# Kernel tuning notes

Measured on AMD Instinct MI355X. Metric: run time of the kernel, lower is better.

The kernel has to match this reference:

```python
import jax, jax.numpy as jnp
import numpy as np
from jax import lax

B = 8; DIM = 256; NH = 8; PATCH = 8; WS = 28; STRIDE = 8; PAD = 14; ORF = 2.0; IMG = 448


def conv2d(x, w, stride, pad, groups=1):
    return lax.conv_general_dilated(
        x, w, (stride, stride), [(pad, pad), (pad, pad)],
        dimension_numbers=('NCHW', 'OIHW', 'NCHW'), feature_group_count=groups)


def ln_ch(x, g, b):
    # LayerNormProxy: LayerNorm over channel dim of NCHW
    m = jnp.mean(x, 1, keepdims=True)
    v = jnp.mean((x - m) ** 2, 1, keepdims=True)
    return (x - m) * lax.rsqrt(v + 1e-5) * g[None, :, None, None] + b[None, :, None, None]


def bilinear_sample(x, grid):
    # x: (N,C,H,W); grid: (N,Hg,Wg,2) in (x,y) order, [-1,1], align_corners=True, zeros padding
    N, C, H, W = x.shape
    gx = (grid[..., 0] + 1.0) * 0.5 * (W - 1)
    gy = (grid[..., 1] + 1.0) * 0.5 * (H - 1)
    x0 = jnp.floor(gx); y0 = jnp.floor(gy)
    x1 = x0 + 1.0; y1 = y0 + 1.0
    wx1 = gx - x0; wx0 = 1.0 - wx1
    wy1 = gy - y0; wy0 = 1.0 - wy1
    xf = x.reshape(N, C, H * W)

    def corner(ix, iy, w):
        valid = (ix >= 0) & (ix <= W - 1) & (iy >= 0) & (iy <= H - 1)
        ii = (jnp.clip(iy, 0, H - 1) * W + jnp.clip(ix, 0, W - 1)).astype(jnp.int32).reshape(N, -1)
        vals = jax.vmap(lambda f, i: f[:, i])(xf, ii)  # (N,C,Hg*Wg)
        return vals * (w * valid).reshape(N, 1, -1)

    out = (corner(x0, y0, wx0 * wy0) + corner(x1, y0, wx1 * wy0)
           + corner(x0, y1, wx0 * wy1) + corner(x1, y1, wx1 * wy1))
    return out.reshape(N, C, grid.shape[1], grid.shape[2])


def setup_inputs() -> dict:
    key = jax.random.key(0)
    ks = jax.random.split(key, 12)
    s = 0.02
    CG = 64
    return {
        'x': jax.random.normal(ks[0], (B, 3, IMG, IMG), jnp.float32),
        'patch_w': jax.random.normal(ks[1], (DIM, 3, PATCH, PATCH), jnp.float32) * s,
        'patch_b': jnp.zeros((DIM,), jnp.float32),
        'ln1_g': jnp.ones((DIM,), jnp.float32),
        'ln1_b': jnp.zeros((DIM,), jnp.float32),
        'wq': jax.random.normal(ks[2], (DIM, DIM), jnp.float32) * s,
        'bq': jnp.zeros((DIM,), jnp.float32),
        'wk': jax.random.normal(ks[3], (DIM, DIM), jnp.float32) * s,
        'bk': jnp.zeros((DIM,), jnp.float32),
        'wv': jax.random.normal(ks[4], (DIM, DIM), jnp.float32) * s,
        'bv': jnp.zeros((DIM,), jnp.float32),
        'wo': jax.random.normal(ks[5], (DIM, DIM), jnp.float32) * s,
        'bo': jnp.zeros((DIM,), jnp.float32),
        'off_dw_w': jax.random.normal(ks[6], (CG, 1, WS, WS), jnp.float32) * s,
        'off_dw_b': jnp.zeros((CG,), jnp.float32),
        'off_ln_g': jnp.ones((CG,), jnp.float32),
        'off_ln_b': jnp.zeros((CG,), jnp.float32),
        'off_pw_w': jax.random.normal(ks[7], (2, CG), jnp.float32) * s,
        'rpe_w1': jax.random.normal(ks[8], (32, 2), jnp.float32) * 0.1,
        'rpe_b1': jnp.zeros((32,), jnp.float32),
        'rpe_w2': jax.random.normal(ks[9], (2, 32), jnp.float32) * 0.1,
    }


def reference(x, patch_w, patch_b, ln1_g, ln1_b, wq, bq, wk, bk, wv, bv, wo, bo,
              off_dw_w, off_dw_b, off_ln_g, off_ln_b, off_pw_w, rpe_w1, rpe_b1, rpe_w2):
    Bn = x.shape[0]
    # patch embedding: Conv2d(3, dim, patch, patch) + LayerNormProxy
    feat = conv2d(x, patch_w, PATCH, 0) + patch_b[None, :, None, None]
    feat = ln_ch(feat, ln1_g, ln1_b)
    H, W = feat.shape[2], feat.shape[3]  # 56, 56
    G = (H // WS) * (W // WS)            # 4 groups
    CG = DIM // G; GH = NH // G; HC = DIM // NH
    # q projection (1x1 conv)
    q = jnp.einsum('oc,bchw->bohw', wq, feat) + bq[None, :, None, None]
    # offset network on per-group query features
    q_off = q.reshape(Bn * G, CG, H, W)
    off = conv2d(q_off, off_dw_w, STRIDE, PAD, groups=CG) + off_dw_b[None, :, None, None]
    off = jax.nn.gelu(ln_ch(off, off_ln_g, off_ln_b), approximate=False)
    off = jnp.einsum('oc,bchw->bohw', off_pw_w, off)   # (B*G, 2, Hk, Wk)
    Hk, Wk = off.shape[2], off.shape[3]
    ns = Hk * Wk
    rng = jnp.array([1.0 / (Hk - 1), 1.0 / (Wk - 1)], off.dtype).reshape(1, 2, 1, 1)
    offset = jnp.tanh(off) * rng * ORF
    offset = jnp.transpose(offset, (0, 2, 3, 1))  # (B*G, Hk, Wk, 2) in (y, x)
    # reference points, normalized to ~[-1, 1]
    ry = jnp.linspace(0.5, Hk - 0.5, Hk) / (Hk - 1) * 2.0 - 1.0
    rx = jnp.linspace(0.5, Wk - 0.5, Wk) / (Wk - 1) * 2.0 - 1.0
    ref = jnp.stack(jnp.meshgrid(ry, rx, indexing='ij'), -1)  # (Hk, Wk, 2)
    ref = jnp.broadcast_to(ref[None], (Bn * G, Hk, Wk, 2))
    pos = offset + ref
    # deformable sampling (grid expects (x, y) order)
    xs = bilinear_sample(feat.reshape(Bn * G, CG, H, W), pos[..., ::-1])  # (B*G, CG, Hk, Wk)
    xs = xs.reshape(Bn, DIM, ns)
    k = jnp.einsum('oc,bcn->bon', wk, xs) + bk[None, :, None]
    v = jnp.einsum('oc,bcn->bon', wv, xs) + bv[None, :, None]
    qh = q.reshape(Bn * NH, HC, H * W)
    kh = k.reshape(Bn * NH, HC, ns)
    vh = v.reshape(Bn * NH, HC, ns)
    attn = jnp.einsum('bcm,bcn->bmn', qh, kh) * (HC ** -0.5)  # (B*NH, HW, ns)
    # log-CPB relative position bias
    qy = jnp.linspace(0.0, float(H), H) / (H - 1) * 2.0 - 1.0
    qx = jnp.linspace(0.0, float(W), W) / (W - 1) * 2.0 - 1.0
    qg = jnp.stack(jnp.meshgrid(qy, qx, indexing='ij'), -1).reshape(H * W, 2)
    disp = (qg[None, :, None, :] - pos.reshape(Bn * G, ns, 2)[:, None, :, :]) * 4.0
    disp = jnp.sign(disp) * jnp.log2(jnp.abs(disp) + 1.0) / 3.0  # /log2(8)
    bias = jax.nn.relu(jnp.einsum('bmnc,hc->bmnh', disp, rpe_w1) + rpe_b1)
    bias = jnp.einsum('bmnh,oh->bmno', bias, rpe_w2)  # (B*G, HW, ns, GH)
    attn = attn + jnp.transpose(bias, (0, 3, 1, 2)).reshape(Bn * NH, H * W, ns)
    attn = jax.nn.softmax(attn, axis=-1)
    out = jnp.einsum('bmn,bcn->bcm', attn, vh).reshape(Bn, DIM, H, W)
    y = jnp.einsum('oc,bchw->bohw', wo, out) + bo[None, :, None, None]
    return (y, pos.reshape(Bn, G, Hk, Wk, 2), ref.reshape(Bn, G, Hk, Wk, 2))
```

## Files before the change

### kernel.cpp

```cpp
#include <hip/hip_runtime.h>
#include <cstddef>


typedef short bf16x8 __attribute__((ext_vector_type(8)));
typedef float f32x4 __attribute__((ext_vector_type(4)));

static __device__ __forceinline__ ushort f2bf(float f) {
  union { float f; unsigned u; } v; v.f = f;
  unsigned r = v.u + 0x7fffu + ((v.u >> 16) & 1u);
  return (ushort)(r >> 16);
}
static __device__ __forceinline__ float bf2f(ushort u) {
  union { unsigned u; float f; } v; v.u = ((unsigned)u) << 16;
  return v.f;
}

#define OFF_FEATB 0u
#define OFF_QPK   3211264u
#define OFF_Q     6422528u
#define OFF_POS   12845056u
#define OFF_XS    12849152u
#define OFF_KPK   12980224u
#define OFF_VPK   13045760u
#define OFF_PWP   13111296u
#define OFF_WQP   13135872u
#define OFF_WOP   13168640u
#define OFF_WKT   13201408u
#define OFF_WVT   13266944u

__global__ __launch_bounds__(256) void k_pack(
    const float* __restrict__ pw, const float* __restrict__ wq,
    const float* __restrict__ wk, const float* __restrict__ wv,
    const float* __restrict__ wo, ushort* __restrict__ pwp,
    ushort* __restrict__ wqp, ushort* __restrict__ wop,
    float* __restrict__ wkT, float* __restrict__ wvT) {
  const int o = blockIdx.x, t = threadIdx.x, m = blockIdx.y;
  if (m == 0) {
    if (t < 192) pwp[((t >> 3) * 256 + o) * 8 + (t & 7)] = f2bf(pw[o * 192 + t]);
  } else if (m == 1) {
    wqp[((t >> 3) * 256 + o) * 8 + (t & 7)] = f2bf(wq[o * 256 + t]);
  } else if (m == 2) {
    wop[((t >> 3) * 256 + o) * 8 + (t & 7)] = f2bf(wo[o * 256 + t]);
  } else if (m == 3) {
    wkT[t * 256 + o] = wk[o * 256 + t];
  } else {
    wvT[t * 256 + o] = wv[o * 256 + t];
  }
}

__global__ __launch_bounds__(256) void k_patch_mfma(
    const float* __restrict__ x, const ushort* __restrict__ pwp,
    const float* __restrict__ pb, const float* __restrict__ g1,
    const float* __restrict__ b1, ushort* __restrict__ featb) {
  const int t = threadIdx.x;
  const int lane = t & 63;
  const int wid = t >> 6;
  const int m_base = blockIdx.x * 64 + wid * 16;
  const int kg = lane >> 4;
  const int lr = lane & 15;
  const int mA = m_base + lr;
  const int bA = mA / 3136;
  const int posA = mA - bA * 3136;
  const int ohA = posA / 56;
  const int owA = posA - ohA * 56;

  f32x4 acc[16];
#pragma unroll
  for (int f = 0; f < 16; f++) {
    float bv = pb[f * 16 + lr];
    acc[f] = (f32x4){bv, bv, bv, bv};
  }
#pragma unroll
  for (int ks = 0; ks < 6; ks++) {
    const int k8 = ks * 4 + kg;
    const int ci = k8 >> 3, ii = k8 & 7;
    const float* xp =
        x + (((size_t)bA * 3 + ci) * 448 + (ohA * 8 + ii)) * 448 + owA * 8;
    float4 v0 = *(const float4*)xp;
    float4 v1 = *(const float4*)(xp + 4);
    bf16x8 a;
    a[0] = (short)f2bf(v0.x); a[1] = (short)f2bf(v0.y);
    a[2] = (short)f2bf(v0.z); a[3] = (short)f2bf(v0.w);
    a[4] = (short)f2bf(v1.x); a[5] = (short)f2bf(v1.y);
    a[6] = (short)f2bf(v1.z); a[7] = (short)f2bf(v1.w);
#pragma unroll
    for (int f = 0; f < 16; f++) {
      bf16x8 bfr = *(const bf16x8*)(pwp + (size_t)(k8 * 256 + f * 16 + lr) * 8);
      acc[f] = __builtin_amdgcn_mfma_f32_16x16x32_bf16(a, bfr, acc[f], 0, 0, 0);
    }
  }
  float mean[4], rstd[4];
#pragma unroll
  for (int j = 0; j < 4; j++) {
    float s1 = 0.f, s2 = 0.f;
#pragma unroll
    for (int f = 0; f < 16; f++) { float v = acc[f][j]; s1 += v; s2 += v * v; }
#pragma unroll
    for (int off = 8; off >= 1; off >>= 1) {
      s1 += __shfl_xor(s1, off);
      s2 += __shfl_xor(s2, off);
    }
    float mn = s1 * (1.f / 256.f);
    float var = s2 * (1.f / 256.f) - mn * mn;
    mean[j] = mn; rstd[j] = rsqrtf(var + 1e-5f);
  }
#pragma unroll
  for (int f = 0; f < 16; f++) {
    const int c = f * 16 + lr;
    const float gg = g1[c], bb = b1[c];
#pragma unroll
    for (int j = 0; j < 4; j++) {
      const int mo = m_base + kg * 4 + j;
      float v = (acc[f][j] - mean[j]) * rstd[j] * gg + bb;
      featb[(size_t)mo * 256 + c] = f2bf(v);
    }
  }
}

__global__ __launch_bounds__(512) void k_gemm_mfma(
    const ushort* __restrict__ apk, const ushort* __restrict__ wp,
    const float* __restrict__ bias, float* __restrict__ out,
    ushort* __restrict__ opk) {
  const int t = threadIdx.x;
  const int lane = t & 63;
  const int wid = t >> 6;
  const int mt = wid >> 1, nh = wid & 1;
  const int lr = lane & 15, kg = lane >> 4;
  const int m_base = blockIdx.x * 64 + mt * 16;
  const int mA = m_base + lr;

  f32x4 acc[8];
#pragma unroll
  for (int f = 0; f < 8; f++) {
    float bv = bias[nh * 128 + f * 16 + lr];
    acc[f] = (f32x4){bv, bv, bv, bv};
  }
  const ushort* arow = apk + (size_t)mA * 256;
#pragma unroll
  for (int ks = 0; ks < 8; ks++) {
    bf16x8 a = *(const bf16x8*)(arow + ks * 32 + kg * 8);
#pragma unroll
    for (int f = 0; f < 8; f++) {
      const int o = nh * 128 + f * 16 + lr;
      bf16x8 bfr = *(const bf16x8*)(wp + (size_t)((ks * 4 + kg) * 256 + o) * 8);
      acc[f] = __builtin_amdgcn_mfma_f32_16x16x32_bf16(a, bfr, acc[f], 0, 0, 0);
    }
  }
  __shared__ float sA[64 * 257];
#pragma unroll
  for (int f = 0; f < 8; f++) {
#pragma unroll
    for (int j = 0; j < 4; j++)
      sA[(mt * 16 + kg * 4 + j) * 257 + nh * 128 + f * 16 + lr] = acc[f][j];
  }
  __syncthreads();
  const int b = (blockIdx.x * 64) / 3136;
  const int pos0 = (blockIdx.x * 64) % 3136;
#pragma unroll
  for (int i = 0; i < 32; i++) {
    int idx = t + i * 512;
    int c = idx >> 6, mm = idx & 63;
    out[((size_t)b * 256 + c) * 3136 + pos0 + mm] = sA[mm * 257 + c];
  }
  if (opk) {
    const int mm = t & 63;
    const int cs = t >> 6;
#pragma unroll
    for (int i = 0; i < 4; i++) {
      int c0 = cs * 32 + i * 8;
      bf16x8 v8;
#pragma unroll
      for (int j = 0; j < 8; j++) v8[j] = (short)f2bf(sA[mm * 257 + c0 + j]);
      *(bf16x8*)(opk + ((size_t)(blockIdx.x * 64 + mm)) * 256 + c0) = v8;
    }
  }
}

__global__ __launch_bounds__(128) void k_offset_conv(
    const float* __restrict__ q, const float* __restrict__ dww,
    float* __restrict__ convo) {
  const int bg = blockIdx.y;
  const int wv = threadIdx.x >> 6;
  const int lane = threadIdx.x & 63;
  const int ch = blockIdx.x * 2 + wv;
  const int b = bg >> 2, g = bg & 3;

  __shared__ float pl[2][7072];
  float* P = pl[wv];
  for (int idx = lane; idx < 7072; idx += 64) P[idx] = 0.f;

  const float* qb = q + ((size_t)b * 256 + g * 64 + ch) * 3136;
  if (lane < 56) {
    for (int r = 0; r < 56; r++) {
      int hr = r + 14;
      P[hr * 84 + (lane + 14) + (hr >> 3)] = qb[r * 56 + lane];
    }
  }
  const int oh = lane >> 3, ow = lane & 7;
  const int chs = __builtin_amdgcn_readfirstlane(ch);
  const float* wr = dww + (size_t)chs * 784;
  float acc = 0.f;
  const int r0 = oh * 8, c0 = ow * 8;
  for (int i = 0; i < 28; i++) {
    int hr = r0 + i;
    const float* prow = P + hr * 84 + c0 + (hr >> 3);
    const float* wrr = wr + i * 28;
#pragma unroll
    for (int j = 0; j < 28; j++)
      acc = fmaf(prow[j], wrr[j], acc);
  }
  convo[bg * 4096 + lane * 64 + ch] = acc;
}

__global__ __launch_bounds__(256) void k_offset_post(
    const float* __restrict__ convo, const float* __restrict__ dwb,
    const float* __restrict__ lng, const float* __restrict__ lnb,
    const float* __restrict__ pww, float* __restrict__ pos_ws,
    float* __restrict__ out_pos, float* __restrict__ out_ref) {
  const int bg = blockIdx.y;
  const int wv = threadIdx.x >> 6;
  const int lane = threadIdx.x & 63;
  const int idx = blockIdx.x * 4 + wv;
  const int oh = idx >> 3, ow = idx & 7;

  float acc = convo[bg * 4096 + idx * 64 + lane] + dwb[lane];

  float s1 = acc, s2 = acc * acc;
#pragma unroll
  for (int off = 32; off >= 1; off >>= 1) {
    s1 += __shfl_xor(s1, off);
    s2 += __shfl_xor(s2, off);
  }
  float m = s1 * (1.f / 64.f);
  float var = s2 * (1.f / 64.f) - m * m;
  float val = (acc - m) * rsqrtf(var + 1e-5f) * lng[lane] + lnb[lane];
  val = 0.5f * val * (1.f + erff(val * 0.70710678118654752f));
  float p0 = pww[lane] * val, p1 = pww[64 + lane] * val;
#pragma unroll
  for (int off = 32; off >= 1; off >>= 1) {
    p0 += __shfl_xor(p0, off);
    p1 += __shfl_xor(p1, off);
  }
  if (lane == 0) {
    float offy = tanhf(p0) * (2.0f / 7.0f);
    float offx = tanhf(p1) * (2.0f / 7.0f);
    float ry = (0.5f + oh) * (2.0f / 7.0f) - 1.0f;
    float rx = (0.5f + ow) * (2.0f / 7.0f) - 1.0f;
    float py = offy + ry, px = offx + rx;
    int o = bg * 128 + idx * 2;
    pos_ws[o] = py;  pos_ws[o + 1] = px;
    out_pos[o] = py; out_pos[o + 1] = px;
    out_ref[o] = ry; out_ref[o + 1] = rx;
  }
}

__global__ __launch_bounds__(256) void k_sample(
    const ushort* __restrict__ featb, const float* __restrict__ pos_ws,
    float* __restrict__ xs) {
  const int bg = blockIdx.y;
  const int wv = threadIdx.x >> 6, lane = threadIdx.x & 63;
  const int n = blockIdx.x * 4 + wv;
  const int b = bg >> 2, g = bg & 3;

  float py = pos_ws[bg * 128 + n * 2];
  float px = pos_ws[bg * 128 + n * 2 + 1];
  float gx = (px + 1.f) * 0.5f * 55.f;
  float gy = (py + 1.f) * 0.5f * 55.f;
  float x0f = floorf(gx), y0f = floorf(gy);
  int x0 = (int)x0f, y0 = (int)y0f;
  float wx1 = gx - x0f, wx0 = 1.f - wx1;
  float wy1 = gy - y0f, wy0 = 1.f - wy1;

  const size_t mb = (size_t)b * 3136;
  const int cofs = g * 64 + lane;
  float acc = 0.f;
  if (x0 >= 0 && x0 <= 55 && y0 >= 0 && y0 <= 55)
    acc = fmaf(bf2f(featb[(mb + y0 * 56 + x0) * 256 + cofs]), wx0 * wy0, acc);
  if (x0 + 1 >= 0 && x0 + 1 <= 55 && y0 >= 0 && y0 <= 55)
    acc = fmaf(bf2f(featb[(mb + y0 * 56 + x0 + 1) * 256 + cofs]), wx1 * wy0, acc);
  if (x0 >= 0 && x0 <= 55 && y0 + 1 >= 0 && y0 + 1 <= 55)
    acc = fmaf(bf2f(featb[(mb + (y0 + 1) * 56 + x0) * 256 + cofs]), wx0 * wy1, acc);
  if (x0 + 1 >= 0 && x0 + 1 <= 55 && y0 + 1 >= 0 && y0 + 1 <= 55)
    acc = fmaf(bf2f(featb[(mb + (y0 + 1) * 56 + x0 + 1) * 256 + cofs]), wx1 * wy1, acc);

  xs[((size_t)bg * 64 + lane) * 64 + n] = acc;
}

__global__ __launch_bounds__(256) void k_kv(
    const float* __restrict__ xs, const float* __restrict__ wkT,
    const float* __restrict__ bk, const float* __restrict__ wvT,
    const float* __restrict__ bv, ushort* __restrict__ kpk,
    ushort* __restrict__ vpk) {
  const int b = blockIdx.y;
  const int n = blockIdx.x;
  const int t = threadIdx.x;
  __shared__ float sxs[256];
  sxs[t] = xs[((size_t)b * 256 + t) * 64 + n];
  __syncthreads();
  float ak = bk[t], av = bv[t];
  for (int c = 0; c < 256; c++) {
    float xv = sxs[c];
    ak = fmaf(wkT[c * 256 + t], xv, ak);
    av = fmaf(wvT[c * 256 + t], xv, av);
  }
  const int h = t >> 5, cc = t & 31;
  const size_t base = (size_t)(b * 8 + h) * 2048;
  kpk[base + (size_t)((cc >> 3) * 64 + n) * 8 + (cc & 7)] = f2bf(ak);
  vpk[base + (size_t)((n >> 3) * 32 + cc) * 8 + (n & 7)] = f2bf(av);
}

__global__ __launch_bounds__(256) void k_attn_mfma(
    const ushort* __restrict__ qpk, const ushort* __restrict__ kpk,
    const ushort* __restrict__ vpk, const float* __restrict__ pos_ws,
    const float* __restrict__ w1, const float* __restrict__ b1,
    const float* __restrict__ w2, ushort* __restrict__ attnpk) {
  const int bg = blockIdx.y;
  const int b = bg >> 2, g = bg & 3;
  const int m0 = blockIdx.x * 64;
  const int t = threadIdx.x;
  const int lane = t & 63, w = t >> 6;

  __shared__ float bias0[64 * 68];
  __shared__ float bias1[64 * 68];
  __shared__ ushort Pbuf[4][16 * 72];
  __shared__ float posl[128];
  __shared__ float4 rpe4[32];
  __shared__ float rpeB[32];

  if (t < 128) posl[t] = pos_ws[bg * 128 + t];
  if (t < 32) {
    rpe4[t] = make_float4(w1[t * 2], w1[t * 2 + 1], b1[t], w2[t]);
    rpeB[t] = w2[32 + t];
  }
  __syncthreads();

  {
    const int i = t >> 2;
    const int n0 = (t & 3) * 16;
    const int m = m0 + i;
    const int my = m / 56, mx = m % 56;
    const float qgy = (float)my * (56.0f / 55.0f) * (2.0f / 55.0f) - 1.0f;
    const float qgx = (float)mx * (56.0f / 55.0f) * (2.0f / 55.0f) - 1.0f;
    float ty[16], tx[16], a0[16], a1[16];
#pragma unroll
    for (int u = 0; u < 16; u++) {
      int n = n0 + u;
      float dy = (qgy - posl[2 * n]) * 4.f;
      float dx = (qgx - posl[2 * n + 1]) * 4.f;
      ty[u] = copysignf(log2f(fabsf(dy) + 1.f) * (1.f / 3.f), dy);
      tx[u] = copysignf(log2f(fabsf(dx) + 1.f) * (1.f / 3.f), dx);
      a0[u] = 0.f; a1[u] = 0.f;
    }
    for (int j = 0; j < 32; j++) {
      float4 r = rpe4[j];
      float wb = rpeB[j];
#pragma unroll
      for (int u = 0; u < 16; u++) {
        float hv = fmaf(r.x, ty[u], fmaf(r.y, tx[u], r.z));
        hv = fmaxf(hv, 0.f);
        a0[u] = fmaf(r.w, hv, a0[u]);
        a1[u] = fmaf(wb, hv, a1[u]);
      }
    }
    float* b0p = bias0 + i * 68 + n0;
    float* b1p = bias1 + i * 68 + n0;
#pragma unroll
    for (int u = 0; u < 16; u++) { b0p[u] = a0[u]; b1p[u] = a1[u]; }
  }

  const int lr = lane & 15, kg = lane >> 4;
  const int mrow = m0 + w * 16 + lr;
  const float scale = 0.17677669529663687f;
  ushort* pb = Pbuf[w];

  f32x4 oacc[2][2];
#pragma unroll
  for (int gh = 0; gh < 2; gh++)
#pragma unroll
    for (int cf = 0; cf < 2; cf++) oacc[gh][cf] = (f32x4){0.f, 0.f, 0.f, 0.f};

#pragma unroll
  for (int gh = 0; gh < 2; gh++) {
    bf16x8 a = *(const bf16x8*)(qpk +
        ((size_t)(b * 3136 + mrow) * 256 + g * 64 + gh * 32 + kg * 8));
    const ushort* kbase = kpk + (size_t)(b * 8 + g * 2 + gh) * 2048;
    f32x4 s[4];
#pragma unroll
    for (int nf = 0; nf < 4; nf++) {
      bf16x8 bfr = *(const bf16x8*)(kbase + (size_t)(kg * 64 + nf * 16 + lr) * 8);
      s[nf] = __builtin_amdgcn_mfma_f32_16x16x32_bf16(
          a, bfr, (f32x4){0.f, 0.f, 0.f, 0.f}, 0, 0, 0);
    }
    const float* bt = gh ? bias1 : bias0;
#pragma unroll
    for (int nf = 0; nf < 4; nf++)
#pragma unroll
      for (int j = 0; j < 4; j++)
        s[nf][j] = fmaf(s[nf][j], scale,
                        bt[(w * 16 + kg * 4 + j) * 68 + nf * 16 + lr]);
#pragma unroll
    for (int j = 0; j < 4; j++) {
      float m1 = fmaxf(fmaxf(s[0][j], s[1][j]), fmaxf(s[2][j], s[3][j]));
#pragma unroll
      for (int o = 8; o >= 1; o >>= 1) m1 = fmaxf(m1, __shfl_xor(m1, o));
      float ss = 0.f;
#pragma unroll
      for (int nf = 0; nf < 4; nf++) {
        float e = __expf(s[nf][j] - m1);
        s[nf][j] = e;
        ss += e;
      }
#pragma unroll
      for (int o = 8; o >= 1; o >>= 1) ss += __shfl_xor(ss, o);
      float inv = 1.f / ss;
#pragma unroll
      for (int nf = 0; nf < 4; nf++) s[nf][j] *= inv;
    }
#pragma unroll
    for (int nf = 0; nf < 4; nf++)
#pragma unroll
      for (int j = 0; j < 4; j++)
        pb[(kg * 4 + j) * 72 + nf * 16 + lr] = f2bf(s[nf][j]);
    const ushort* vbase = vpk + (size_t)(b * 8 + g * 2 + gh) * 2048;
#pragma unroll
    for (int ks = 0; ks < 2; ks++) {
      bf16x8 pa = *(const bf16x8*)(pb + lr * 72 + ks * 32 + kg * 8);
#pragma unroll
      for (int cf = 0; cf < 2; cf++) {
        bf16x8 vb = *(const bf16x8*)(vbase +
            (size_t)((ks * 4 + kg) * 32 + cf * 16 + lr) * 8);
        oacc[gh][cf] = __builtin_amdgcn_mfma_f32_16x16x32_bf16(
            pa, vb, oacc[gh][cf], 0, 0, 0);
      }
    }
  }

  ushort* outb = (ushort*)bias0;
#pragma unroll
  for (int gh = 0; gh < 2; gh++)
#pragma unroll
    for (int cf = 0; cf < 2; cf++)
#pragma unroll
      for (int j = 0; j < 4; j++)
        outb[(w * 16 + kg * 4 + j) * 136 + gh * 32 + cf * 16 + lr] =
            f2bf(oacc[gh][cf][j]);
  __syncthreads();
#pragma unroll
  for (int r2 = 0; r2 < 2; r2++) {
    int row = (t >> 3) + r2 * 32;
    int chunk = t & 7;
    bf16x8 v8 = *(const bf16x8*)(outb + row * 136 + chunk * 8);
    *(bf16x8*)(attnpk +
               ((size_t)(b * 3136 + m0 + row) * 256 + g * 64 + chunk * 8)) = v8;
  }
}

extern "C" void kernel_launch(void* const* d_in, const int* in_sizes, int n_in,
                              void* d_out, int out_size, void* d_ws,
                              size_t ws_size, hipStream_t stream) {
  const float* x       = (const float*)d_in[0];
  const float* patch_w = (const float*)d_in[1];
  const float* patch_b = (const float*)d_in[2];
  const float* ln1_g   = (const float*)d_in[3];
  const float* ln1_b   = (const float*)d_in[4];
  const float* wq      = (const float*)d_in[5];
  const float* bq      = (const float*)d_in[6];
  const float* wk      = (const float*)d_in[7];
  const float* bk      = (const float*)d_in[8];
  const float* wv      = (const float*)d_in[9];
  const float* bv      = (const float*)d_in[10];
  const float* wo      = (const float*)d_in[11];
  const float* bo      = (const float*)d_in[12];
  const float* off_dw_w = (const float*)d_in[13];
  const float* off_dw_b = (const float*)d_in[14];
  const float* off_ln_g = (const float*)d_in[15];
  const float* off_ln_b = (const float*)d_in[16];
  const float* off_pw_w = (const float*)d_in[17];
  const float* rpe_w1  = (const float*)d_in[18];
  const float* rpe_b1  = (const float*)d_in[19];
  const float* rpe_w2  = (const float*)d_in[20];

  float* ws = (float*)d_ws;
  ushort* featb = (ushort*)(ws + OFF_FEATB);
  ushort* attnpk = featb;
  ushort* qpk = (ushort*)(ws + OFF_QPK);
  float* q    = ws + OFF_Q;
  float* posw = ws + OFF_POS;
  float* xs   = ws + OFF_XS;
  float* convo = ws + OFF_XS;
  ushort* kpk = (ushort*)(ws + OFF_KPK);
  ushort* vpk = (ushort*)(ws + OFF_VPK);
  ushort* pwp = (ushort*)(ws + OFF_PWP);
  ushort* wqp = (ushort*)(ws + OFF_WQP);
  ushort* wop = (ushort*)(ws + OFF_WOP);
  float* wkT  = ws + OFF_WKT;
  float* wvT  = ws + OFF_WVT;

  float* y = (float*)d_out;
  float* out_pos = y + 6422528;
  float* out_ref = out_pos + 4096;

  hipLaunchKernelGGL(k_pack, dim3(256, 5), dim3(256), 0, stream,
                     patch_w, wq, wk, wv, wo, pwp, wqp, wop, wkT, wvT);
  hipLaunchKernelGGL(k_patch_mfma, dim3(392), dim3(256), 0, stream,
                     x, pwp, patch_b, ln1_g, ln1_b, featb);
  hipLaunchKernelGGL(k_gemm_mfma, dim3(392), dim3(512), 0, stream,
                     featb, wqp, bq, q, qpk);
  hipLaunchKernelGGL(k_offset_conv, dim3(32, 32), dim3(128), 0, stream,
                     q, off_dw_w, convo);
  hipLaunchKernelGGL(k_offset_post, dim3(16, 32), dim3(256), 0, stream,
                     convo, off_dw_b, off_ln_g, off_ln_b, off_pw_w,
                     posw, out_pos, out_ref);
  hipLaunchKernelGGL(k_sample, dim3(16, 32), dim3(256), 0, stream,
                     featb, posw, xs);
  hipLaunchKernelGGL(k_kv, dim3(64, 8), dim3(256), 0, stream,
                     xs, wkT, bk, wvT, bv, kpk, vpk);
  hipLaunchKernelGGL(k_attn_mfma, dim3(49, 32), dim3(256), 0, stream,
                     qpk, kpk, vpk, posw, rpe_w1, rpe_b1, rpe_w2, attnpk);
  hipLaunchKernelGGL(k_gemm_mfma, dim3(392), dim3(512), 0, stream,
                     attnpk, wop, bo, y, (ushort*)nullptr);
}
```

Before: 240.0 us.

## Pre-convert input to bf16, fuse sampling into KV, compute RPE bias in registers

Three changes. A new pass converts the fp32 input image to bf16 once, so the patch-embed kernel reads half the bytes and drops its per-tile conversion, at the cost of an extra kernel plus a full write and read of the bf16 copy. The bilinear sampling kernel is merged into the K/V projection kernel, which removes the xs round trip through global memory and one launch. The attention kernel now computes the log-CPB bias in MFMA-fragment layout in registers with fast log2 instead of staging it in LDS, which cuts shared memory use but raises register pressure.

```diff
diff --git a/kernel.cpp b/kernel.cpp
--- a/kernel.cpp
+++ b/kernel.cpp
@@ -27,6 +27,19 @@
 #define OFF_WOP   13168640u
 #define OFF_WKT   13201408u
 #define OFF_WVT   13266944u
+
+__global__ __launch_bounds__(256) void k_xcvt(
+    const float* __restrict__ x, ushort* __restrict__ xb) {
+  const size_t i0 = ((size_t)blockIdx.x * 256 + threadIdx.x) * 8;
+  float4 v0 = *(const float4*)(x + i0);
+  float4 v1 = *(const float4*)(x + i0 + 4);
+  bf16x8 o;
+  o[0] = (short)f2bf(v0.x); o[1] = (short)f2bf(v0.y);
+  o[2] = (short)f2bf(v0.z); o[3] = (short)f2bf(v0.w);
+  o[4] = (short)f2bf(v1.x); o[5] = (short)f2bf(v1.y);
+  o[6] = (short)f2bf(v1.z); o[7] = (short)f2bf(v1.w);
+  *(bf16x8*)(xb + i0) = o;
+}
 
 __global__ __launch_bounds__(256) void k_pack(
     const float* __restrict__ pw, const float* __restrict__ wq,
@@ -49,7 +62,7 @@
 }
 
 __global__ __launch_bounds__(256) void k_patch_mfma(
-    const float* __restrict__ x, const ushort* __restrict__ pwp,
+    const ushort* __restrict__ xb, const ushort* __restrict__ pwp,
     const float* __restrict__ pb, const float* __restrict__ g1,
     const float* __restrict__ b1, ushort* __restrict__ featb) {
   const int t = threadIdx.x;
@@ -74,15 +87,8 @@
   for (int ks = 0; ks < 6; ks++) {
     const int k8 = ks * 4 + kg;
     const int ci = k8 >> 3, ii = k8 & 7;
-    const float* xp =
-        x + (((size_t)bA * 3 + ci) * 448 + (ohA * 8 + ii)) * 448 + owA * 8;
-    float4 v0 = *(const float4*)xp;
-    float4 v1 = *(const float4*)(xp + 4);
-    bf16x8 a;
-    a[0] = (short)f2bf(v0.x); a[1] = (short)f2bf(v0.y);
-    a[2] = (short)f2bf(v0.z); a[3] = (short)f2bf(v0.w);
-    a[4] = (short)f2bf(v1.x); a[5] = (short)f2bf(v1.y);
-    a[6] = (short)f2bf(v1.z); a[7] = (short)f2bf(v1.w);
+    bf16x8 a = *(const bf16x8*)(xb +
+        (((size_t)bA * 3 + ci) * 448 + (ohA * 8 + ii)) * 448 + owA * 8);
 #pragma unroll
     for (int f = 0; f < 16; f++) {
       bf16x8 bfr = *(const bf16x8*)(pwp + (size_t)(k8 * 256 + f * 16 + lr) * 8);
@@ -254,49 +260,42 @@
   }
 }
 
-__global__ __launch_bounds__(256) void k_sample(
+__global__ __launch_bounds__(256) void k_sample_kv(
     const ushort* __restrict__ featb, const float* __restrict__ pos_ws,
-    float* __restrict__ xs) {
-  const int bg = blockIdx.y;
-  const int wv = threadIdx.x >> 6, lane = threadIdx.x & 63;
-  const int n = blockIdx.x * 4 + wv;
-  const int b = bg >> 2, g = bg & 3;
-
-  float py = pos_ws[bg * 128 + n * 2];
-  float px = pos_ws[bg * 128 + n * 2 + 1];
-  float gx = (px + 1.f) * 0.5f * 55.f;
-  float gy = (py + 1.f) * 0.5f * 55.f;
-  float x0f = floorf(gx), y0f = floorf(gy);
-  int x0 = (int)x0f, y0 = (int)y0f;
-  float wx1 = gx - x0f, wx0 = 1.f - wx1;
-  float wy1 = gy - y0f, wy0 = 1.f - wy1;
-
-  const size_t mb = (size_t)b * 3136;
-  const int cofs = g * 64 + lane;
-  float acc = 0.f;
-  if (x0 >= 0 && x0 <= 55 && y0 >= 0 && y0 <= 55)
-    acc = fmaf(bf2f(featb[(mb + y0 * 56 + x0) * 256 + cofs]), wx0 * wy0, acc);
-  if (x0 + 1 >= 0 && x0 + 1 <= 55 && y0 >= 0 && y0 <= 55)
-    acc = fmaf(bf2f(featb[(mb + y0 * 56 + x0 + 1) * 256 + cofs]), wx1 * wy0, acc);
-  if (x0 >= 0 && x0 <= 55 && y0 + 1 >= 0 && y0 + 1 <= 55)
-    acc = fmaf(bf2f(featb[(mb + (y0 + 1) * 56 + x0) * 256 + cofs]), wx0 * wy1, acc);
-  if (x0 + 1 >= 0 && x0 + 1 <= 55 && y0 + 1 >= 0 && y0 + 1 <= 55)
-    acc = fmaf(bf2f(featb[(mb + (y0 + 1) * 56 + x0 + 1) * 256 + cofs]), wx1 * wy1, acc);
-
-  xs[((size_t)bg * 64 + lane) * 64 + n] = acc;
-}
-
-__global__ __launch_bounds__(256) void k_kv(
-    const float* __restrict__ xs, const float* __restrict__ wkT,
-    const float* __restrict__ bk, const float* __restrict__ wvT,
-    const float* __restrict__ bv, ushort* __restrict__ kpk,
-    ushort* __restrict__ vpk) {
+    const float* __restrict__ wkT, const float* __restrict__ bk,
+    const float* __restrict__ wvT, const float* __restrict__ bv,
+    ushort* __restrict__ kpk, ushort* __restrict__ vpk) {
   const int b = blockIdx.y;
   const int n = blockIdx.x;
   const int t = threadIdx.x;
+  const int g = t >> 6, lane = t & 63;
+  const int bg = b * 4 + g;
+
   __shared__ float sxs[256];
-  sxs[t] = xs[((size_t)b * 256 + t) * 64 + n];
+  {
+    float py = pos_ws[bg * 128 + n * 2];
+    float px = pos_ws[bg * 128 + n * 2 + 1];
+    float gx = (px + 1.f) * 0.5f * 55.f;
+    float gy = (py + 1.f) * 0.5f * 55.f;
+    float x0f = floorf(gx), y0f = floorf(gy);
+    int x0 = (int)x0f, y0 = (int)y0f;
+    float wx1 = gx - x0f, wx0 = 1.f - wx1;
+    float wy1 = gy - y0f, wy0 = 1.f - wy1;
+    const size_t mb = (size_t)b * 3136;
+    const int cofs = g * 64 + lane;
+    float acc = 0.f;
+    if (x0 >= 0 && x0 <= 55 && y0 >= 0 && y0 <= 55)
+      acc = fmaf(bf2f(featb[(mb + y0 * 56 + x0) * 256 + cofs]), wx0 * wy0, acc);
+    if (x0 + 1 >= 0 && x0 + 1 <= 55 && y0 >= 0 && y0 <= 55)
+      acc = fmaf(bf2f(featb[(mb + y0 * 56 + x0 + 1) * 256 + cofs]), wx1 * wy0, acc);
+    if (x0 >= 0 && x0 <= 55 && y0 + 1 >= 0 && y0 + 1 <= 55)
+      acc = fmaf(bf2f(featb[(mb + (y0 + 1) * 56 + x0) * 256 + cofs]), wx0 * wy1, acc);
+    if (x0 + 1 >= 0 && x0 + 1 <= 55 && y0 + 1 >= 0 && y0 + 1 <= 55)
+      acc = fmaf(bf2f(featb[(mb + (y0 + 1) * 56 + x0 + 1) * 256 + cofs]), wx1 * wy1, acc);
+    sxs[g * 64 + lane] = acc;
+  }
   __syncthreads();
+
   float ak = bk[t], av = bv[t];
   for (int c = 0; c < 256; c++) {
     float xv = sxs[c];
@@ -319,10 +318,10 @@
   const int m0 = blockIdx.x * 64;
   const int t = threadIdx.x;
   const int lane = t & 63, w = t >> 6;
-
-  __shared__ float bias0[64 * 68];
-  __shared__ float bias1[64 * 68];
+  const int lr = lane & 15, kg = lane >> 4;
+
   __shared__ ushort Pbuf[4][16 * 72];
+  __shared__ ushort outb[64 * 72];
   __shared__ float posl[128];
   __shared__ float4 rpe4[32];
   __shared__ float rpeB[32];
@@ -334,41 +333,41 @@
   }
   __syncthreads();
 
-  {
-    const int i = t >> 2;
-    const int n0 = (t & 3) * 16;
-    const int m = m0 + i;
-    const int my = m / 56, mx = m % 56;
-    const float qgy = (float)my * (56.0f / 55.0f) * (2.0f / 55.0f) - 1.0f;
-    const float qgx = (float)mx * (56.0f / 55.0f) * (2.0f / 55.0f) - 1.0f;
-    float ty[16], tx[16], a0[16], a1[16];
-#pragma unroll
-    for (int u = 0; u < 16; u++) {
-      int n = n0 + u;
-      float dy = (qgy - posl[2 * n]) * 4.f;
-      float dx = (qgx - posl[2 * n + 1]) * 4.f;
-      ty[u] = copysignf(log2f(fabsf(dy) + 1.f) * (1.f / 3.f), dy);
-      tx[u] = copysignf(log2f(fabsf(dx) + 1.f) * (1.f / 3.f), dx);
-      a0[u] = 0.f; a1[u] = 0.f;
-    }
-    for (int j = 0; j < 32; j++) {
-      float4 r = rpe4[j];
-      float wb = rpeB[j];
-#pragma unroll
-      for (int u = 0; u < 16; u++) {
-        float hv = fmaf(r.x, ty[u], fmaf(r.y, tx[u], r.z));
-        hv = fmaxf(hv, 0.f);
-        a0[u] = fmaf(r.w, hv, a0[u]);
-        a1[u] = fmaf(wb, hv, a1[u]);
-      }
-    }
-    float* b0p = bias0 + i * 68 + n0;
-    float* b1p = bias1 + i * 68 + n0;
-#pragma unroll
-    for (int u = 0; u < 16; u++) { b0p[u] = a0[u]; b1p[u] = a1[u]; }
-  }
-
-  const int lr = lane & 15, kg = lane >> 4;
+  float qgy[4], qgx[4];
+#pragma unroll
+  for (int j = 0; j < 4; j++) {
+    int m = m0 + w * 16 + kg * 4 + j;
+    int my = m / 56, mx = m % 56;
+    qgy[j] = (float)my * (56.0f / 55.0f) * (2.0f / 55.0f) - 1.0f;
+    qgx[j] = (float)mx * (56.0f / 55.0f) * (2.0f / 55.0f) - 1.0f;
+  }
+  float tyv[16], txv[16];
+#pragma unroll
+  for (int nf = 0; nf < 4; nf++) {
+    int n = nf * 16 + lr;
+    float py = posl[2 * n], px = posl[2 * n + 1];
+#pragma unroll
+    for (int j = 0; j < 4; j++) {
+      float dy = (qgy[j] - py) * 4.f;
+      float dx = (qgx[j] - px) * 4.f;
+      tyv[nf * 4 + j] = copysignf(__log2f(fabsf(dy) + 1.f) * (1.f / 3.f), dy);
+      txv[nf * 4 + j] = copysignf(__log2f(fabsf(dx) + 1.f) * (1.f / 3.f), dx);
+    }
+  }
+  float bb0[16], bb1[16];
+#pragma unroll
+  for (int p = 0; p < 16; p++) { bb0[p] = 0.f; bb1[p] = 0.f; }
+  for (int jj = 0; jj < 32; jj++) {
+    float4 r = rpe4[jj];
+    float wb = rpeB[jj];
+#pragma unroll
+    for (int p = 0; p < 16; p++) {
+      float hv = fmaxf(fmaf(r.x, tyv[p], fmaf(r.y, txv[p], r.z)), 0.f);
+      bb0[p] = fmaf(r.w, hv, bb0[p]);
+      bb1[p] = fmaf(wb, hv, bb1[p]);
+    }
+  }
+
   const int mrow = m0 + w * 16 + lr;
   const float scale = 0.17677669529663687f;
   ushort* pb = Pbuf[w];
@@ -391,13 +390,12 @@
       s[nf] = __builtin_amdgcn_mfma_f32_16x16x32_bf16(
           a, bfr, (f32x4){0.f, 0.f, 0.f, 0.f}, 0, 0, 0);
     }
-    const float* bt = gh ? bias1 : bias0;
 #pragma unroll
     for (int nf = 0; nf < 4; nf++)
 #pragma unroll
       for (int j = 0; j < 4; j++)
         s[nf][j] = fmaf(s[nf][j], scale,
-                        bt[(w * 16 + kg * 4 + j) * 68 + nf * 16 + lr]);
+                        gh ? bb1[nf * 4 + j] : bb0[nf * 4 + j]);
 #pragma unroll
     for (int j = 0; j < 4; j++) {
       float m1 = fmaxf(fmaxf(s[0][j], s[1][j]), fmaxf(s[2][j], s[3][j]));
@@ -435,21 +433,20 @@
     }
   }
 
-  ushort* outb = (ushort*)bias0;
 #pragma unroll
   for (int gh = 0; gh < 2; gh++)
 #pragma unroll
     for (int cf = 0; cf < 2; cf++)
 #pragma unroll
       for (int j = 0; j < 4; j++)
-        outb[(w * 16 + kg * 4 + j) * 136 + gh * 32 + cf * 16 + lr] =
+        outb[(w * 16 + kg * 4 + j) * 72 + gh * 32 + cf * 16 + lr] =
             f2bf(oacc[gh][cf][j]);
   __syncthreads();
 #pragma unroll
   for (int r2 = 0; r2 < 2; r2++) {
     int row = (t >> 3) + r2 * 32;
     int chunk = t & 7;
-    bf16x8 v8 = *(const bf16x8*)(outb + row * 136 + chunk * 8);
+    bf16x8 v8 = *(const bf16x8*)(outb + row * 72 + chunk * 8);
     *(bf16x8*)(attnpk +
                ((size_t)(b * 3136 + m0 + row) * 256 + g * 64 + chunk * 8)) = v8;
   }
@@ -485,8 +482,8 @@
   ushort* attnpk = featb;
   ushort* qpk = (ushort*)(ws + OFF_QPK);
   float* q    = ws + OFF_Q;
+  ushort* xb  = (ushort*)(ws + OFF_Q);
   float* posw = ws + OFF_POS;
-  float* xs   = ws + OFF_XS;
   float* convo = ws + OFF_XS;
   ushort* kpk = (ushort*)(ws + OFF_KPK);
   ushort* vpk = (ushort*)(ws + OFF_VPK);
@@ -500,10 +497,11 @@
   float* out_pos = y + 6422528;
   float* out_ref = out_pos + 4096;
 
+  hipLaunchKernelGGL(k_xcvt, dim3(2352), dim3(256), 0, stream, x, xb);
   hipLaunchKernelGGL(k_pack, dim3(256, 5), dim3(256), 0, stream,
                      patch_w, wq, wk, wv, wo, pwp, wqp, wop, wkT, wvT);
   hipLaunchKernelGGL(k_patch_mfma, dim3(392), dim3(256), 0, stream,
-                     x, pwp, patch_b, ln1_g, ln1_b, featb);
+                     xb, pwp, patch_b, ln1_g, ln1_b, featb);
   hipLaunchKernelGGL(k_gemm_mfma, dim3(392), dim3(512), 0, stream,
                      featb, wqp, bq, q, qpk);
   hipLaunchKernelGGL(k_offset_conv, dim3(32, 32), dim3(128), 0, stream,
@@ -511,10 +509,8 @@
   hipLaunchKernelGGL(k_offset_post, dim3(16, 32), dim3(256), 0, stream,
                      convo, off_dw_b, off_ln_g, off_ln_b, off_pw_w,
                      posw, out_pos, out_ref);
-  hipLaunchKernelGGL(k_sample, dim3(16, 32), dim3(256), 0, stream,
-                     featb, posw, xs);
-  hipLaunchKernelGGL(k_kv, dim3(64, 8), dim3(256), 0, stream,
-                     xs, wkT, bk, wvT, bv, kpk, vpk);
+  hipLaunchKernelGGL(k_sample_kv, dim3(64, 8), dim3(256), 0, stream,
+                     featb, posw, wkT, bk, wvT, bv, kpk, vpk);
   hipLaunchKernelGGL(k_attn_mfma, dim3(49, 32), dim3(256), 0, stream,
                      qpk, kpk, vpk, posw, rpe_w1, rpe_b1, rpe_w2, attnpk);
   hipLaunchKernelGGL(k_gemm_mfma, dim3(392), dim3(512), 0, stream,
```

Result: no change. 244.0 us (+1.7%).
